# Kernel optimization log

Measured on AMD Instinct MI355X. Metric: run time of the kernel, lower is better.

The kernel has to match this reference:

```python
import jax, jax.numpy as jnp
import numpy as np

N_NODES = 50000
HIDDEN = 64
N_EDGES = 800000
HOPS = (1, 2, 3)


def setup_inputs() -> dict:
    key = jax.random.key(0)
    ks = jax.random.split(key, 16)
    d = HIDDEN
    inp = {
        "x": jax.random.normal(ks[0], (N_NODES, d), dtype=jnp.float32),
        "edge_index": jax.random.randint(ks[1], (2, N_EDGES), 0, N_NODES, dtype=jnp.int64),
    }
    s = 1.0 / np.sqrt(d)
    # per-hop GIN MLP params: Linear(d,d) -> ReLU -> Linear(d,d)
    for i in range(len(HOPS)):
        inp[f"W1_{i}"] = jax.random.uniform(ks[2 + 4 * i], (d, d), jnp.float32, -s, s)
        inp[f"b1_{i}"] = jax.random.uniform(ks[3 + 4 * i], (d,), jnp.float32, -s, s)
        inp[f"W2_{i}"] = jax.random.uniform(ks[4 + 4 * i], (d, d), jnp.float32, -s, s)
        inp[f"b2_{i}"] = jax.random.uniform(ks[5 + 4 * i], (d,), jnp.float32, -s, s)
    so = 1.0 / np.sqrt(d * len(HOPS))
    inp["Wo"] = jax.random.uniform(ks[14], (d * len(HOPS), d), jnp.float32, -so, so)
    inp["bo"] = jax.random.uniform(ks[15], (d,), jnp.float32, -so, so)
    return inp


def _gin_conv(h, src, dst, W1, b1, W2, b2):
    # GINConv with eps=0: MLP(x + sum_{j in N(i)} x_j)
    agg = jax.ops.segment_sum(h[src], dst, num_segments=N_NODES)  # [N, d]
    z = h + agg
    z = jax.nn.relu(z @ W1 + b1) @ W2 + b2
    return z


def reference(x, edge_index,
              W1_0, b1_0, W2_0, b2_0,
              W1_1, b1_1, W2_1, b2_1,
              W1_2, b1_2, W2_2, b2_2,
              Wo, bo):
    src, dst = edge_index[0], edge_index[1]
    params = [(W1_0, b1_0, W2_0, b2_0),
              (W1_1, b1_1, W2_1, b2_1),
              (W1_2, b1_2, W2_2, b2_2)]
    outs = []
    for hop, (W1, b1, W2, b2) in zip(HOPS, params):
        h = x
        for _ in range(hop):
            h = _gin_conv(h, src, dst, W1, b1, W2, b2)
        outs.append(h)
    return jnp.concatenate(outs, axis=-1) @ Wo + bo
```

## Files before the change

kernel.cpp:

```cpp
#include <hip/hip_runtime.h>

#define NN 50000
#define NE 800000
#define D  64
#define TILE 64
#define TPB 512
#define NBLK 196


__global__ __launch_bounds__(256) void k_count(const int* __restrict__ ei, int* __restrict__ deg) {
    int e = blockIdx.x * 256 + threadIdx.x;
    if (e < NE) atomicAdd(&deg[ei[NE + e]], 1);
}

__global__ __launch_bounds__(256) void k_scan2(const int* __restrict__ deg,
                                               int* __restrict__ row_ptr,
                                               int* __restrict__ cursor) {
    __shared__ int s[256];
    __shared__ int sboff;
    int t = threadIdx.x;
    int b = blockIdx.x;

    int lim = b * 256;
    int pacc = 0;
    for (int i = t; i < lim; i += 256) pacc += deg[i];
    s[t] = pacc;
    __syncthreads();
    for (int off = 128; off > 0; off >>= 1) {
        if (t < off) s[t] += s[t + off];
        __syncthreads();
    }
    if (t == 0) sboff = s[0];
    __syncthreads();
    int boffv = sboff;
    __syncthreads();

    int i = lim + t;
    int v = (i < NN) ? deg[i] : 0;
    s[t] = v;
    __syncthreads();
    for (int off = 1; off < 256; off <<= 1) {
        int u = (t >= off) ? s[t - off] : 0;
        __syncthreads();
        s[t] += u;
        __syncthreads();
    }
    int excl = s[t] - v + boffv;
    if (i < NN) { row_ptr[i] = excl; cursor[i] = excl; }
    if (b == 0 && t == 0) row_ptr[NN] = NE;
}

__global__ __launch_bounds__(256) void k_fill(const int* __restrict__ ei,
                                              int* __restrict__ cursor,
                                              int* __restrict__ colv) {
    int e = blockIdx.x * 256 + threadIdx.x;
    if (e < NE) {
        int d = ei[NE + e];
        int p = atomicAdd(&cursor[d], 1);
        colv[p] = ei[e];
    }
}


__device__ __forceinline__ float4 gather_row(const float4* __restrict__ h4,
                                             const int* __restrict__ row_ptr,
                                             const int* __restrict__ colv,
                                             int n, int g, int q) {
    float4 a0 = make_float4(0.f, 0.f, 0.f, 0.f);
    float4 a1 = make_float4(0.f, 0.f, 0.f, 0.f);
    float4 a2 = make_float4(0.f, 0.f, 0.f, 0.f);
    float4 a3 = make_float4(0.f, 0.f, 0.f, 0.f);
    if (n >= 0) {
        if (g == 0) a0 = h4[n * 16 + q];
        int e1 = row_ptr[n + 1];
        int e  = row_ptr[n] + g;
        for (; e + 12 < e1; e += 16) {
            int s0 = colv[e], s1 = colv[e + 4], s2 = colv[e + 8], s3 = colv[e + 12];
            float4 v0 = h4[s0 * 16 + q];
            float4 v1 = h4[s1 * 16 + q];
            float4 v2 = h4[s2 * 16 + q];
            float4 v3 = h4[s3 * 16 + q];
            a0.x += v0.x; a0.y += v0.y; a0.z += v0.z; a0.w += v0.w;
            a1.x += v1.x; a1.y += v1.y; a1.z += v1.z; a1.w += v1.w;
            a2.x += v2.x; a2.y += v2.y; a2.z += v2.z; a2.w += v2.w;
            a3.x += v3.x; a3.y += v3.y; a3.z += v3.z; a3.w += v3.w;
        }
        for (; e < e1; e += 4) {
            float4 v = h4[colv[e] * 16 + q];
            a1.x += v.x; a1.y += v.y; a1.z += v.z; a1.w += v.w;
        }
        a0.x += a1.x + a2.x + a3.x;
        a0.y += a1.y + a2.y + a3.y;
        a0.z += a1.z + a2.z + a3.z;
        a0.w += a1.w + a2.w + a3.w;
    }
    a0.x += __shfl_xor(a0.x, 16); a0.y += __shfl_xor(a0.y, 16);
    a0.z += __shfl_xor(a0.z, 16); a0.w += __shfl_xor(a0.w, 16);
    a0.x += __shfl_xor(a0.x, 32); a0.y += __shfl_xor(a0.y, 32);
    a0.z += __shfl_xor(a0.z, 32); a0.w += __shfl_xor(a0.w, 32);
    return a0;
}


__device__ __forceinline__ void conv_body(
    const float4* __restrict__ h4,
    const int* __restrict__ row_ptr,
    const int* __restrict__ colv,
    const float* __restrict__ W1, const float* __restrict__ b1,
    const float* __restrict__ W2, const float* __restrict__ b2,
    float4* __restrict__ out4,
    float (&sW)[D][D], float4 (&sZ4)[TILE][17], float* sB1, float* sB2,
    int node0)
{
    int tid = threadIdx.x;

    {
        const float4* w14 = (const float4*)W1;
        float4* s14 = (float4*)sW;
        for (int i = tid; i < D * D / 4; i += TPB) s14[i] = w14[i];
        if (tid < D) { sB1[tid] = b1[tid]; sB2[tid] = b2[tid]; }
    }

    int wave = tid >> 6, lane = tid & 63;
    int g = lane >> 4, q = lane & 15;

    for (int r = wave; r < TILE; r += (TPB / 64)) {
        int n = node0 + r;
        float4 a = gather_row(h4, row_ptr, colv, (n < NN) ? n : -1, g, q);
        if (g == 0) sZ4[r][q] = a;
    }
    __syncthreads();

    int tr = tid >> 4, tc = tid & 15;
    float* zr0 = (float*)&sZ4[tr * 2 + 0][0];
    float* zr1 = (float*)&sZ4[tr * 2 + 1][0];

    float acc[2][4];
    #pragma unroll
    for (int c = 0; c < 4; ++c) { acc[0][c] = sB1[tc * 4 + c]; acc[1][c] = sB1[tc * 4 + c]; }
    #pragma unroll 16
    for (int k = 0; k < D; ++k) {
        float z0 = zr0[k], z1 = zr1[k];
        #pragma unroll
        for (int c = 0; c < 4; ++c) {
            float w = sW[k][tc * 4 + c];
            acc[0][c] += z0 * w;
            acc[1][c] += z1 * w;
        }
    }
    {
        float4 h0, h1;
        h0.x = fmaxf(acc[0][0], 0.f); h0.y = fmaxf(acc[0][1], 0.f);
        h0.z = fmaxf(acc[0][2], 0.f); h0.w = fmaxf(acc[0][3], 0.f);
        h1.x = fmaxf(acc[1][0], 0.f); h1.y = fmaxf(acc[1][1], 0.f);
        h1.z = fmaxf(acc[1][2], 0.f); h1.w = fmaxf(acc[1][3], 0.f);
        *(float4*)&zr0[tc * 4] = h0;
        *(float4*)&zr1[tc * 4] = h1;
    }
    __syncthreads();

    {
        const float4* w24 = (const float4*)W2;
        float4* s24 = (float4*)sW;
        for (int i = tid; i < D * D / 4; i += TPB) s24[i] = w24[i];
    }
    __syncthreads();

    #pragma unroll
    for (int c = 0; c < 4; ++c) { acc[0][c] = sB2[tc * 4 + c]; acc[1][c] = sB2[tc * 4 + c]; }
    #pragma unroll 16
    for (int k = 0; k < D; ++k) {
        float z0 = zr0[k], z1 = zr1[k];
        #pragma unroll
        for (int c = 0; c < 4; ++c) {
            float w = sW[k][tc * 4 + c];
            acc[0][c] += z0 * w;
            acc[1][c] += z1 * w;
        }
    }
    #pragma unroll
    for (int i = 0; i < 2; ++i) {
        int n = node0 + tr * 2 + i;
        if (n < NN) {
            float4 o;
            o.x = acc[i][0]; o.y = acc[i][1]; o.z = acc[i][2]; o.w = acc[i][3];
            out4[n * 16 + tc] = o;
        }
    }
}

__global__ __launch_bounds__(TPB, 8) void k_conv_dual(
    const float4* __restrict__ hA4, const float4* __restrict__ hB4,
    const int* __restrict__ row_ptr,
    const int* __restrict__ colv,
    const float* __restrict__ W1a, const float* __restrict__ b1a,
    const float* __restrict__ W2a, const float* __restrict__ b2a,
    const float* __restrict__ W1b, const float* __restrict__ b1b,
    const float* __restrict__ W2b, const float* __restrict__ b2b,
    float4* __restrict__ outA4, float4* __restrict__ outB4, int nb)
{
    __shared__ float sW[D][D];
    __shared__ float4 sZ4[TILE][17];
    __shared__ float sB1[D], sB2[D];
    int b = blockIdx.x;
    if (b < nb) {
        conv_body(hA4, row_ptr, colv, W1a, b1a, W2a, b2a, outA4,
                  sW, sZ4, sB1, sB2, b * TILE);
    } else {
        conv_body(hB4, row_ptr, colv, W1b, b1b, W2b, b2b, outB4,
                  sW, sZ4, sB1, sB2, (b - nb) * TILE);
    }
}


__global__ __launch_bounds__(TPB, 8) void k_conv_last(
    const float4* __restrict__ h4,
    const float4* __restrict__ H0, const float4* __restrict__ H1,
    const int* __restrict__ row_ptr, const int* __restrict__ colv,
    const float* __restrict__ W1, const float* __restrict__ b1,
    const float* __restrict__ W2, const float* __restrict__ b2,
    const float* __restrict__ Wo, const float* __restrict__ bo,
    float4* __restrict__ out4)
{
    __shared__ float sW[D][D];
    __shared__ float4 sZ4[TILE][17];
    __shared__ float sB1[D], sB2[D];

    int tid = threadIdx.x;
    int node0 = blockIdx.x * TILE;

    {
        const float4* w14 = (const float4*)W1;
        float4* s14 = (float4*)sW;
        for (int i = tid; i < D * D / 4; i += TPB) s14[i] = w14[i];
        if (tid < D) { sB1[tid] = b1[tid]; sB2[tid] = b2[tid]; }
    }

    int wave = tid >> 6, lane = tid & 63;
    int g = lane >> 4, q = lane & 15;

    for (int r = wave; r < TILE; r += (TPB / 64)) {
        int n = node0 + r;
        float4 a = gather_row(h4, row_ptr, colv, (n < NN) ? n : -1, g, q);
        if (g == 0) sZ4[r][q] = a;
    }
    __syncthreads();

    int tr = tid >> 4, tc = tid & 15;
    float* zr0 = (float*)&sZ4[tr * 2 + 0][0];
    float* zr1 = (float*)&sZ4[tr * 2 + 1][0];

    float acc[2][4];
    #pragma unroll
    for (int c = 0; c < 4; ++c) { acc[0][c] = sB1[tc * 4 + c]; acc[1][c] = sB1[tc * 4 + c]; }
    #pragma unroll 16
    for (int k = 0; k < D; ++k) {
        float z0 = zr0[k], z1 = zr1[k];
        #pragma unroll
        for (int c = 0; c < 4; ++c) {
            float w = sW[k][tc * 4 + c];
            acc[0][c] += z0 * w;
            acc[1][c] += z1 * w;
        }
    }
    {
        float4 h0, h1;
        h0.x = fmaxf(acc[0][0], 0.f); h0.y = fmaxf(acc[0][1], 0.f);
        h0.z = fmaxf(acc[0][2], 0.f); h0.w = fmaxf(acc[0][3], 0.f);
        h1.x = fmaxf(acc[1][0], 0.f); h1.y = fmaxf(acc[1][1], 0.f);
        h1.z = fmaxf(acc[1][2], 0.f); h1.w = fmaxf(acc[1][3], 0.f);
        *(float4*)&zr0[tc * 4] = h0;
        *(float4*)&zr1[tc * 4] = h1;
    }
    __syncthreads();

    {
        const float4* w24 = (const float4*)W2;
        float4* s24 = (float4*)sW;
        for (int i = tid; i < D * D / 4; i += TPB) s24[i] = w24[i];
    }
    __syncthreads();

    #pragma unroll
    for (int c = 0; c < 4; ++c) { acc[0][c] = sB2[tc * 4 + c]; acc[1][c] = sB2[tc * 4 + c]; }
    #pragma unroll 16
    for (int k = 0; k < D; ++k) {
        float z0 = zr0[k], z1 = zr1[k];
        #pragma unroll
        for (int c = 0; c < 4; ++c) {
            float w = sW[k][tc * 4 + c];
            acc[0][c] += z0 * w;
            acc[1][c] += z1 * w;
        }
    }
    {
        float4 h0, h1;
        h0.x = acc[0][0]; h0.y = acc[0][1]; h0.z = acc[0][2]; h0.w = acc[0][3];
        h1.x = acc[1][0]; h1.y = acc[1][1]; h1.z = acc[1][2]; h1.w = acc[1][3];
        *(float4*)&zr0[tc * 4] = h0;
        *(float4*)&zr1[tc * 4] = h1;
    }
    __syncthreads();

    float accO[2][4];
    int n0 = node0 + tr * 2 + 0;
    int n1 = node0 + tr * 2 + 1;

    #pragma unroll 1
    for (int m = 0; m < 3; ++m) {
        {
            const float4* w4 = (const float4*)(Wo + m * 64 * D);
            float4* s4 = (float4*)sW;
            for (int i = tid; i < D * D / 4; i += TPB) s4[i] = w4[i];
        }
        __syncthreads();

        if (m == 0) {
            #pragma unroll
            for (int c = 0; c < 4; ++c) { accO[0][c] = sB1[0] * 0.f; }
            #pragma unroll
            for (int c = 0; c < 4; ++c) { accO[0][c] = bo[tc * 4 + c]; accO[1][c] = accO[0][c]; }
        }

        if (m < 2) {
            const float4* Hc = (m == 0) ? H0 : H1;
            #pragma unroll 4
            for (int k4 = 0; k4 < 16; ++k4) {
                float4 z0v = Hc[n0 * 16 + k4];
                float4 z1v = Hc[n1 * 16 + k4];
                #pragma unroll
                for (int j = 0; j < 4; ++j) {
                    int k = k4 * 4 + j;
                    float z0 = (j == 0) ? z0v.x : (j == 1) ? z0v.y : (j == 2) ? z0v.z : z0v.w;
                    float z1 = (j == 0) ? z1v.x : (j == 1) ? z1v.y : (j == 2) ? z1v.z : z1v.w;
                    #pragma unroll
                    for (int c = 0; c < 4; ++c) {
                        float w = sW[k][tc * 4 + c];
                        accO[0][c] += z0 * w;
                        accO[1][c] += z1 * w;
                    }
                }
            }
        } else {
            #pragma unroll 16
            for (int k = 0; k < D; ++k) {
                float z0 = zr0[k], z1 = zr1[k];
                #pragma unroll
                for (int c = 0; c < 4; ++c) {
                    float w = sW[k][tc * 4 + c];
                    accO[0][c] += z0 * w;
                    accO[1][c] += z1 * w;
                }
            }
        }
        if (m < 2) __syncthreads();
    }

    #pragma unroll
    for (int i = 0; i < 2; ++i) {
        int n = node0 + tr * 2 + i;
        if (n < NN) {
            float4 o;
            o.x = accO[i][0]; o.y = accO[i][1]; o.z = accO[i][2]; o.w = accO[i][3];
            out4[n * 16 + tc] = o;
        }
    }
}


__global__ __launch_bounds__(TPB) void k_aggmlp3(
    const float4* __restrict__ h4,
    const int* __restrict__ row_ptr,
    const int* __restrict__ colv,
    const float* __restrict__ W1a, const float* __restrict__ b1a,
    const float* __restrict__ W2a, const float* __restrict__ b2a,
    const float* __restrict__ W1b, const float* __restrict__ b1b,
    const float* __restrict__ W2b, const float* __restrict__ b2b,
    const float* __restrict__ W1c, const float* __restrict__ b1c,
    const float* __restrict__ W2c, const float* __restrict__ b2c,
    float4* __restrict__ outA, float4* __restrict__ outB, float4* __restrict__ outC)
{
    __shared__ float sW[D][D];
    __shared__ float4 sZ4[TILE][17];
    __shared__ float4 sH4[TILE][17];
    __shared__ float sB[D];

    int tid = threadIdx.x;
    int node0 = blockIdx.x * TILE;

    int wave = tid >> 6, lane = tid & 63;
    int g = lane >> 4, q = lane & 15;

    for (int r = wave; r < TILE; r += (TPB / 64)) {
        int n = node0 + r;
        float4 a = gather_row(h4, row_ptr, colv, (n < NN) ? n : -1, g, q);
        if (g == 0) sZ4[r][q] = a;
    }

    int tr = tid >> 4, tc = tid & 15;
    float* zr0 = (float*)&sZ4[tr * 2 + 0][0];
    float* zr1 = (float*)&sZ4[tr * 2 + 1][0];
    float* hr0 = (float*)&sH4[tr * 2 + 0][0];
    float* hr1 = (float*)&sH4[tr * 2 + 1][0];

    #pragma unroll 1
    for (int m = 0; m < 3; ++m) {
        const float* W1 = (m == 0) ? W1a : (m == 1) ? W1b : W1c;
        const float* B1 = (m == 0) ? b1a : (m == 1) ? b1b : b1c;
        const float* W2 = (m == 0) ? W2a : (m == 1) ? W2b : W2c;
        const float* B2 = (m == 0) ? b2a : (m == 1) ? b2b : b2c;
        float4* out4 = (m == 0) ? outA : (m == 1) ? outB : outC;

        {
            const float4* w4 = (const float4*)W1;
            float4* s4 = (float4*)sW;
            for (int i = tid; i < D * D / 4; i += TPB) s4[i] = w4[i];
            if (tid < D) sB[tid] = B1[tid];
        }
        __syncthreads();

        float acc[2][4];
        #pragma unroll
        for (int c = 0; c < 4; ++c) { acc[0][c] = sB[tc * 4 + c]; acc[1][c] = sB[tc * 4 + c]; }
        #pragma unroll 16
        for (int k = 0; k < D; ++k) {
            float z0 = zr0[k], z1 = zr1[k];
            #pragma unroll
            for (int c = 0; c < 4; ++c) {
                float w = sW[k][tc * 4 + c];
                acc[0][c] += z0 * w;
                acc[1][c] += z1 * w;
            }
        }
        {
            float4 h0, h1;
            h0.x = fmaxf(acc[0][0], 0.f); h0.y = fmaxf(acc[0][1], 0.f);
            h0.z = fmaxf(acc[0][2], 0.f); h0.w = fmaxf(acc[0][3], 0.f);
            h1.x = fmaxf(acc[1][0], 0.f); h1.y = fmaxf(acc[1][1], 0.f);
            h1.z = fmaxf(acc[1][2], 0.f); h1.w = fmaxf(acc[1][3], 0.f);
            *(float4*)&hr0[tc * 4] = h0;
            *(float4*)&hr1[tc * 4] = h1;
        }
        __syncthreads();

        {
            const float4* w4 = (const float4*)W2;
            float4* s4 = (float4*)sW;
            for (int i = tid; i < D * D / 4; i += TPB) s4[i] = w4[i];
            if (tid < D) sB[tid] = B2[tid];
        }
        __syncthreads();

        #pragma unroll
        for (int c = 0; c < 4; ++c) { acc[0][c] = sB[tc * 4 + c]; acc[1][c] = sB[tc * 4 + c]; }
        #pragma unroll 16
        for (int k = 0; k < D; ++k) {
            float h0 = hr0[k], h1 = hr1[k];
            #pragma unroll
            for (int c = 0; c < 4; ++c) {
                float w = sW[k][tc * 4 + c];
                acc[0][c] += h0 * w;
                acc[1][c] += h1 * w;
            }
        }
        #pragma unroll
        for (int i = 0; i < 2; ++i) {
            int n = node0 + tr * 2 + i;
            if (n < NN) {
                float4 o;
                o.x = acc[i][0]; o.y = acc[i][1]; o.z = acc[i][2]; o.w = acc[i][3];
                out4[n * 16 + tc] = o;
            }
        }
        __syncthreads();
    }
}


extern "C" void kernel_launch(void* const* d_in, const int* in_sizes, int n_in,
                              void* d_out, int out_size, void* d_ws, size_t ws_size,
                              hipStream_t stream) {
    const float* x    = (const float*)d_in[0];
    const int*   ei   = (const int*)d_in[1];
    const float* W1_0 = (const float*)d_in[2];
    const float* b1_0 = (const float*)d_in[3];
    const float* W2_0 = (const float*)d_in[4];
    const float* b2_0 = (const float*)d_in[5];
    const float* W1_1 = (const float*)d_in[6];
    const float* b1_1 = (const float*)d_in[7];
    const float* W2_1 = (const float*)d_in[8];
    const float* b2_1 = (const float*)d_in[9];
    const float* W1_2 = (const float*)d_in[10];
    const float* b1_2 = (const float*)d_in[11];
    const float* W2_2 = (const float*)d_in[12];
    const float* b2_2 = (const float*)d_in[13];
    const float* Wo   = (const float*)d_in[14];
    const float* bo   = (const float*)d_in[15];
    float4* out = (float4*)d_out;

    char* ws = (char*)d_ws;
    int* deg     = (int*)(ws + 0);
    int* cursor  = (int*)(ws + 200704);
    int* row_ptr = (int*)(ws + 401408);
    int* colv    = (int*)(ws + 602112);
    float* fbase = (float*)(ws + 3804160);
    float4* H0  = (float4*)(fbase);
    float4* H1  = (float4*)(fbase + 3200000);
    float4* tB  = (float4*)(fbase + 6400000);
    float4* tC2 = (float4*)(fbase + 9600000);
    const float4* x4 = (const float4*)x;

    hipMemsetAsync(deg, 0, NN * sizeof(int), stream);
    k_count<<<(NE + 255) / 256, 256, 0, stream>>>(ei, deg);
    k_scan2<<<NBLK, 256, 0, stream>>>(deg, row_ptr, cursor);
    k_fill <<<(NE + 255) / 256, 256, 0, stream>>>(ei, cursor, colv);

    int nb = (NN + TILE - 1) / TILE;

    k_aggmlp3<<<nb, TPB, 0, stream>>>(x4, row_ptr, colv,
                                      W1_0, b1_0, W2_0, b2_0,
                                      W1_1, b1_1, W2_1, b2_1,
                                      W1_2, b1_2, W2_2, b2_2,
                                      H0, tB, out);

    k_conv_dual<<<2 * nb, TPB, 0, stream>>>(
        (const float4*)tB, (const float4*)out, row_ptr, colv,
        W1_1, b1_1, W2_1, b2_1,
        W1_2, b1_2, W2_2, b2_2,
        H1, tC2, nb);

    k_conv_last<<<nb, TPB, 0, stream>>>((const float4*)tC2,
                                        (const float4*)H0, (const float4*)H1,
                                        row_ptr, colv,
                                        W1_2, b1_2, W2_2, b2_2,
                                        Wo, bo, out);
}
```

Measured before the change: 371.4 us.

## Fuse whole MixHop pipeline into one cooperative persistent kernel with grid syncs

Replaces the multi-kernel sequence (degree count, scan, fill, aggregation+MLP, dual conv, last conv) with a single cooperative launch of 782 blocks that separates the phases with grid.sync(). This removes per-kernel launch gaps and lets the CSR build and the three hops run inside one resident grid. It keeps a fallback to separate kernels, which now split the last conv and the output projection into k_conv and k_final. It depends on all 782 blocks of 512 threads fitting co-resident; if they do not, the cooperative launch fails and the fallback runs. The fused path also adds full-grid barriers, extra round trips of the aggregated features through global memory, and a first-hop MLP whose three weight sets run serially per block.

New measurement: 1.007 ms. 171% more time.

```diff
diff --git a/kernel.cpp b/kernel.cpp
--- a/kernel.cpp
+++ b/kernel.cpp
@@ -1,65 +1,16 @@
 #include <hip/hip_runtime.h>
+#include <hip/hip_cooperative_groups.h>
+
+namespace cg = cooperative_groups;
 
 #define NN 50000
 #define NE 800000
 #define D  64
 #define TILE 64
 #define TPB 512
+#define NBG 782
+#define NSB 98
 #define NBLK 196
-
-
-__global__ __launch_bounds__(256) void k_count(const int* __restrict__ ei, int* __restrict__ deg) {
-    int e = blockIdx.x * 256 + threadIdx.x;
-    if (e < NE) atomicAdd(&deg[ei[NE + e]], 1);
-}
-
-__global__ __launch_bounds__(256) void k_scan2(const int* __restrict__ deg,
-                                               int* __restrict__ row_ptr,
-                                               int* __restrict__ cursor) {
-    __shared__ int s[256];
-    __shared__ int sboff;
-    int t = threadIdx.x;
-    int b = blockIdx.x;
-
-    int lim = b * 256;
-    int pacc = 0;
-    for (int i = t; i < lim; i += 256) pacc += deg[i];
-    s[t] = pacc;
-    __syncthreads();
-    for (int off = 128; off > 0; off >>= 1) {
-        if (t < off) s[t] += s[t + off];
-        __syncthreads();
-    }
-    if (t == 0) sboff = s[0];
-    __syncthreads();
-    int boffv = sboff;
-    __syncthreads();
-
-    int i = lim + t;
-    int v = (i < NN) ? deg[i] : 0;
-    s[t] = v;
-    __syncthreads();
-    for (int off = 1; off < 256; off <<= 1) {
-        int u = (t >= off) ? s[t - off] : 0;
-        __syncthreads();
-        s[t] += u;
-        __syncthreads();
-    }
-    int excl = s[t] - v + boffv;
-    if (i < NN) { row_ptr[i] = excl; cursor[i] = excl; }
-    if (b == 0 && t == 0) row_ptr[NN] = NE;
-}
-
-__global__ __launch_bounds__(256) void k_fill(const int* __restrict__ ei,
-                                              int* __restrict__ cursor,
-                                              int* __restrict__ colv) {
-    int e = blockIdx.x * 256 + threadIdx.x;
-    if (e < NE) {
-        int d = ei[NE + e];
-        int p = atomicAdd(&cursor[d], 1);
-        colv[p] = ei[e];
-    }
-}
 
 
 __device__ __forceinline__ float4 gather_row(const float4* __restrict__ h4,
@@ -187,6 +138,301 @@
             out4[n * 16 + tc] = o;
         }
     }
+    __syncthreads();
+}
+
+
+__global__ __launch_bounds__(TPB, 8) void k_mixhop(
+    const float4* __restrict__ x4, const int* __restrict__ ei,
+    const float* __restrict__ W1_0, const float* __restrict__ b1_0,
+    const float* __restrict__ W2_0, const float* __restrict__ b2_0,
+    const float* __restrict__ W1_1, const float* __restrict__ b1_1,
+    const float* __restrict__ W2_1, const float* __restrict__ b2_1,
+    const float* __restrict__ W1_2, const float* __restrict__ b1_2,
+    const float* __restrict__ W2_2, const float* __restrict__ b2_2,
+    const float* __restrict__ Wo, const float* __restrict__ bo,
+    float4* __restrict__ out,
+    int* __restrict__ deg, int* __restrict__ cursor,
+    int* __restrict__ row_ptr, int* __restrict__ colv,
+    float4* __restrict__ H0, float4* __restrict__ H1,
+    float4* __restrict__ tB, float4* __restrict__ tC2)
+{
+    cg::grid_group grid = cg::this_grid();
+
+    __shared__ float sW[D][D];
+    __shared__ float4 sZ4[TILE][17];
+    __shared__ float sB1[D], sB2[D];
+
+    int tid = threadIdx.x;
+    int b = blockIdx.x;
+    int gsize = NBG * TPB;
+    int gtid = b * TPB + tid;
+    int node0 = b * TILE;
+
+    for (int i = gtid; i < NN; i += gsize) deg[i] = 0;
+    if (gtid == 0) row_ptr[NN] = NE;
+    grid.sync();
+
+    for (int e = gtid; e < NE; e += gsize) atomicAdd(&deg[ei[NE + e]], 1);
+    grid.sync();
+
+    if (b < NSB) {
+        int* s = (int*)sW;
+        int lim = b * TPB;
+        int pacc = 0;
+        for (int i = tid; i < lim; i += TPB) pacc += deg[i];
+        s[tid] = pacc;
+        __syncthreads();
+        for (int off = 256; off > 0; off >>= 1) {
+            if (tid < off) s[tid] += s[tid + off];
+            __syncthreads();
+        }
+        if (tid == 0) s[TPB] = s[0];
+        __syncthreads();
+        int boffv = s[TPB];
+        __syncthreads();
+
+        int i = lim + tid;
+        int v = (i < NN) ? deg[i] : 0;
+        s[tid] = v;
+        __syncthreads();
+        for (int off = 1; off < TPB; off <<= 1) {
+            int u = (tid >= off) ? s[tid - off] : 0;
+            __syncthreads();
+            s[tid] += u;
+            __syncthreads();
+        }
+        int excl = s[tid] - v + boffv;
+        if (i < NN) { row_ptr[i] = excl; cursor[i] = excl; }
+    }
+    grid.sync();
+
+    for (int e = gtid; e < NE; e += gsize) {
+        int dd = ei[NE + e];
+        int p = atomicAdd(&cursor[dd], 1);
+        colv[p] = ei[e];
+    }
+    grid.sync();
+
+    {
+        int wave = tid >> 6, lane = tid & 63;
+        int g = lane >> 4, q = lane & 15;
+        for (int r = wave; r < TILE; r += (TPB / 64)) {
+            int n = node0 + r;
+            float4 a = gather_row(x4, row_ptr, colv, (n < NN) ? n : -1, g, q);
+            if (g == 0 && n < NN) tC2[n * 16 + q] = a;
+        }
+    }
+    grid.sync();
+
+    {
+        int tr = tid >> 4, tc = tid & 15;
+        float* zr0 = (float*)&sZ4[tr * 2 + 0][0];
+        float* zr1 = (float*)&sZ4[tr * 2 + 1][0];
+
+        #pragma unroll 1
+        for (int m = 0; m < 3; ++m) {
+            const float* W1 = (m == 0) ? W1_0 : (m == 1) ? W1_1 : W1_2;
+            const float* B1 = (m == 0) ? b1_0 : (m == 1) ? b1_1 : b1_2;
+            const float* W2 = (m == 0) ? W2_0 : (m == 1) ? W2_1 : W2_2;
+            const float* B2 = (m == 0) ? b2_0 : (m == 1) ? b2_1 : b2_2;
+            float4* o4      = (m == 0) ? H0   : (m == 1) ? tB   : out;
+
+            {
+                const float4* w4 = (const float4*)W1;
+                float4* s4 = (float4*)sW;
+                for (int i = tid; i < D * D / 4; i += TPB) s4[i] = w4[i];
+                if (tid < D) { sB1[tid] = B1[tid]; sB2[tid] = B2[tid]; }
+            }
+            for (int i = tid; i < TILE * 16; i += TPB) {
+                int r = i >> 4, qq = i & 15;
+                int n = node0 + r;
+                sZ4[r][qq] = (n < NN) ? tC2[n * 16 + qq] : make_float4(0.f, 0.f, 0.f, 0.f);
+            }
+            __syncthreads();
+
+            float acc[2][4];
+            #pragma unroll
+            for (int c = 0; c < 4; ++c) { acc[0][c] = sB1[tc * 4 + c]; acc[1][c] = sB1[tc * 4 + c]; }
+            #pragma unroll 16
+            for (int k = 0; k < D; ++k) {
+                float z0 = zr0[k], z1 = zr1[k];
+                #pragma unroll
+                for (int c = 0; c < 4; ++c) {
+                    float w = sW[k][tc * 4 + c];
+                    acc[0][c] += z0 * w;
+                    acc[1][c] += z1 * w;
+                }
+            }
+            {
+                float4 h0, h1;
+                h0.x = fmaxf(acc[0][0], 0.f); h0.y = fmaxf(acc[0][1], 0.f);
+                h0.z = fmaxf(acc[0][2], 0.f); h0.w = fmaxf(acc[0][3], 0.f);
+                h1.x = fmaxf(acc[1][0], 0.f); h1.y = fmaxf(acc[1][1], 0.f);
+                h1.z = fmaxf(acc[1][2], 0.f); h1.w = fmaxf(acc[1][3], 0.f);
+                *(float4*)&zr0[tc * 4] = h0;
+                *(float4*)&zr1[tc * 4] = h1;
+            }
+            __syncthreads();
+
+            {
+                const float4* w4 = (const float4*)W2;
+                float4* s4 = (float4*)sW;
+                for (int i = tid; i < D * D / 4; i += TPB) s4[i] = w4[i];
+            }
+            __syncthreads();
+
+            #pragma unroll
+            for (int c = 0; c < 4; ++c) { acc[0][c] = sB2[tc * 4 + c]; acc[1][c] = sB2[tc * 4 + c]; }
+            #pragma unroll 16
+            for (int k = 0; k < D; ++k) {
+                float z0 = zr0[k], z1 = zr1[k];
+                #pragma unroll
+                for (int c = 0; c < 4; ++c) {
+                    float w = sW[k][tc * 4 + c];
+                    acc[0][c] += z0 * w;
+                    acc[1][c] += z1 * w;
+                }
+            }
+            #pragma unroll
+            for (int i = 0; i < 2; ++i) {
+                int n = node0 + tr * 2 + i;
+                if (n < NN) {
+                    float4 o;
+                    o.x = acc[i][0]; o.y = acc[i][1]; o.z = acc[i][2]; o.w = acc[i][3];
+                    o4[n * 16 + tc] = o;
+                }
+            }
+            __syncthreads();
+        }
+    }
+    grid.sync();
+
+    conv_body(tB,  row_ptr, colv, W1_1, b1_1, W2_1, b2_1, H1,  sW, sZ4, sB1, sB2, node0);
+    conv_body(out, row_ptr, colv, W1_2, b1_2, W2_2, b2_2, tC2, sW, sZ4, sB1, sB2, node0);
+    grid.sync();
+
+    conv_body(tC2, row_ptr, colv, W1_2, b1_2, W2_2, b2_2, tB, sW, sZ4, sB1, sB2, node0);
+    grid.sync();
+
+    {
+        int tr = tid >> 4, tc = tid & 15;
+        const float* yr0 = (const float*)&sZ4[tr * 2 + 0][0];
+        const float* yr1 = (const float*)&sZ4[tr * 2 + 1][0];
+        float accO[2][4];
+
+        #pragma unroll 1
+        for (int m = 0; m < 3; ++m) {
+            const float4* Hc = (m == 0) ? H0 : (m == 1) ? H1 : tB;
+            {
+                const float4* w4 = (const float4*)(Wo + m * 64 * D);
+                float4* s4 = (float4*)sW;
+                for (int i = tid; i < D * D / 4; i += TPB) s4[i] = w4[i];
+                if (m == 0 && tid < D) sB1[tid] = bo[tid];
+            }
+            for (int i = tid; i < TILE * 16; i += TPB) {
+                int r = i >> 4, qq = i & 15;
+                int n = node0 + r;
+                sZ4[r][qq] = (n < NN) ? Hc[n * 16 + qq] : make_float4(0.f, 0.f, 0.f, 0.f);
+            }
+            __syncthreads();
+
+            if (m == 0) {
+                #pragma unroll
+                for (int c = 0; c < 4; ++c) { accO[0][c] = sB1[tc * 4 + c]; accO[1][c] = sB1[tc * 4 + c]; }
+            }
+            #pragma unroll 16
+            for (int k = 0; k < D; ++k) {
+                float z0 = yr0[k], z1 = yr1[k];
+                #pragma unroll
+                for (int c = 0; c < 4; ++c) {
+                    float w = sW[k][tc * 4 + c];
+                    accO[0][c] += z0 * w;
+                    accO[1][c] += z1 * w;
+                }
+            }
+            __syncthreads();
+        }
+
+        #pragma unroll
+        for (int i = 0; i < 2; ++i) {
+            int n = node0 + tr * 2 + i;
+            if (n < NN) {
+                float4 o;
+                o.x = accO[i][0]; o.y = accO[i][1]; o.z = accO[i][2]; o.w = accO[i][3];
+                out[n * 16 + tc] = o;
+            }
+        }
+    }
+}
+
+
+__global__ __launch_bounds__(256) void k_count(const int* __restrict__ ei, int* __restrict__ deg) {
+    int e = blockIdx.x * 256 + threadIdx.x;
+    if (e < NE) atomicAdd(&deg[ei[NE + e]], 1);
+}
+
+__global__ __launch_bounds__(256) void k_scan2(const int* __restrict__ deg,
+                                               int* __restrict__ row_ptr,
+                                               int* __restrict__ cursor) {
+    __shared__ int s[256];
+    __shared__ int sboff;
+    int t = threadIdx.x;
+    int b = blockIdx.x;
+
+    int lim = b * 256;
+    int pacc = 0;
+    for (int i = t; i < lim; i += 256) pacc += deg[i];
+    s[t] = pacc;
+    __syncthreads();
+    for (int off = 128; off > 0; off >>= 1) {
+        if (t < off) s[t] += s[t + off];
+        __syncthreads();
+    }
+    if (t == 0) sboff = s[0];
+    __syncthreads();
+    int boffv = sboff;
+    __syncthreads();
+
+    int i = lim + t;
+    int v = (i < NN) ? deg[i] : 0;
+    s[t] = v;
+    __syncthreads();
+    for (int off = 1; off < 256; off <<= 1) {
+        int u = (t >= off) ? s[t - off] : 0;
+        __syncthreads();
+        s[t] += u;
+        __syncthreads();
+    }
+    int excl = s[t] - v + boffv;
+    if (i < NN) { row_ptr[i] = excl; cursor[i] = excl; }
+    if (b == 0 && t == 0) row_ptr[NN] = NE;
+}
+
+__global__ __launch_bounds__(256) void k_fill(const int* __restrict__ ei,
+                                              int* __restrict__ cursor,
+                                              int* __restrict__ colv) {
+    int e = blockIdx.x * 256 + threadIdx.x;
+    if (e < NE) {
+        int d = ei[NE + e];
+        int p = atomicAdd(&cursor[d], 1);
+        colv[p] = ei[e];
+    }
+}
+
+__global__ __launch_bounds__(TPB, 8) void k_conv(
+    const float4* __restrict__ h4,
+    const int* __restrict__ row_ptr,
+    const int* __restrict__ colv,
+    const float* __restrict__ W1, const float* __restrict__ b1,
+    const float* __restrict__ W2, const float* __restrict__ b2,
+    float4* __restrict__ out4)
+{
+    __shared__ float sW[D][D];
+    __shared__ float4 sZ4[TILE][17];
+    __shared__ float sB1[D], sB2[D];
+    conv_body(h4, row_ptr, colv, W1, b1, W2, b2, out4,
+              sW, sZ4, sB1, sB2, blockIdx.x * TILE);
 }
 
 __global__ __launch_bounds__(TPB, 8) void k_conv_dual(
@@ -212,162 +458,6 @@
     }
 }
 
-
-__global__ __launch_bounds__(TPB, 8) void k_conv_last(
-    const float4* __restrict__ h4,
-    const float4* __restrict__ H0, const float4* __restrict__ H1,
-    const int* __restrict__ row_ptr, const int* __restrict__ colv,
-    const float* __restrict__ W1, const float* __restrict__ b1,
-    const float* __restrict__ W2, const float* __restrict__ b2,
-    const float* __restrict__ Wo, const float* __restrict__ bo,
-    float4* __restrict__ out4)
-{
-    __shared__ float sW[D][D];
-    __shared__ float4 sZ4[TILE][17];
-    __shared__ float sB1[D], sB2[D];
-
-    int tid = threadIdx.x;
-    int node0 = blockIdx.x * TILE;
-
-    {
-        const float4* w14 = (const float4*)W1;
-        float4* s14 = (float4*)sW;
-        for (int i = tid; i < D * D / 4; i += TPB) s14[i] = w14[i];
-        if (tid < D) { sB1[tid] = b1[tid]; sB2[tid] = b2[tid]; }
-    }
-
-    int wave = tid >> 6, lane = tid & 63;
-    int g = lane >> 4, q = lane & 15;
-
-    for (int r = wave; r < TILE; r += (TPB / 64)) {
-        int n = node0 + r;
-        float4 a = gather_row(h4, row_ptr, colv, (n < NN) ? n : -1, g, q);
-        if (g == 0) sZ4[r][q] = a;
-    }
-    __syncthreads();
-
-    int tr = tid >> 4, tc = tid & 15;
-    float* zr0 = (float*)&sZ4[tr * 2 + 0][0];
-    float* zr1 = (float*)&sZ4[tr * 2 + 1][0];
-
-    float acc[2][4];
-    #pragma unroll
-    for (int c = 0; c < 4; ++c) { acc[0][c] = sB1[tc * 4 + c]; acc[1][c] = sB1[tc * 4 + c]; }
-    #pragma unroll 16
-    for (int k = 0; k < D; ++k) {
-        float z0 = zr0[k], z1 = zr1[k];
-        #pragma unroll
-        for (int c = 0; c < 4; ++c) {
-            float w = sW[k][tc * 4 + c];
-            acc[0][c] += z0 * w;
-            acc[1][c] += z1 * w;
-        }
-    }
-    {
-        float4 h0, h1;
-        h0.x = fmaxf(acc[0][0], 0.f); h0.y = fmaxf(acc[0][1], 0.f);
-        h0.z = fmaxf(acc[0][2], 0.f); h0.w = fmaxf(acc[0][3], 0.f);
-        h1.x = fmaxf(acc[1][0], 0.f); h1.y = fmaxf(acc[1][1], 0.f);
-        h1.z = fmaxf(acc[1][2], 0.f); h1.w = fmaxf(acc[1][3], 0.f);
-        *(float4*)&zr0[tc * 4] = h0;
-        *(float4*)&zr1[tc * 4] = h1;
-    }
-    __syncthreads();
-
-    {
-        const float4* w24 = (const float4*)W2;
-        float4* s24 = (float4*)sW;
-        for (int i = tid; i < D * D / 4; i += TPB) s24[i] = w24[i];
-    }
-    __syncthreads();
-
-    #pragma unroll
-    for (int c = 0; c < 4; ++c) { acc[0][c] = sB2[tc * 4 + c]; acc[1][c] = sB2[tc * 4 + c]; }
-    #pragma unroll 16
-    for (int k = 0; k < D; ++k) {
-        float z0 = zr0[k], z1 = zr1[k];
-        #pragma unroll
-        for (int c = 0; c < 4; ++c) {
-            float w = sW[k][tc * 4 + c];
-            acc[0][c] += z0 * w;
-            acc[1][c] += z1 * w;
-        }
-    }
-    {
-        float4 h0, h1;
-        h0.x = acc[0][0]; h0.y = acc[0][1]; h0.z = acc[0][2]; h0.w = acc[0][3];
-        h1.x = acc[1][0]; h1.y = acc[1][1]; h1.z = acc[1][2]; h1.w = acc[1][3];
-        *(float4*)&zr0[tc * 4] = h0;
-        *(float4*)&zr1[tc * 4] = h1;
-    }
-    __syncthreads();
-
-    float accO[2][4];
-    int n0 = node0 + tr * 2 + 0;
-    int n1 = node0 + tr * 2 + 1;
-
-    #pragma unroll 1
-    for (int m = 0; m < 3; ++m) {
-        {
-            const float4* w4 = (const float4*)(Wo + m * 64 * D);
-            float4* s4 = (float4*)sW;
-            for (int i = tid; i < D * D / 4; i += TPB) s4[i] = w4[i];
-        }
-        __syncthreads();
-
-        if (m == 0) {
-            #pragma unroll
-            for (int c = 0; c < 4; ++c) { accO[0][c] = sB1[0] * 0.f; }
-            #pragma unroll
-            for (int c = 0; c < 4; ++c) { accO[0][c] = bo[tc * 4 + c]; accO[1][c] = accO[0][c]; }
-        }
-
-        if (m < 2) {
-            const float4* Hc = (m == 0) ? H0 : H1;
-            #pragma unroll 4
-            for (int k4 = 0; k4 < 16; ++k4) {
-                float4 z0v = Hc[n0 * 16 + k4];
-                float4 z1v = Hc[n1 * 16 + k4];
-                #pragma unroll
-                for (int j = 0; j < 4; ++j) {
-                    int k = k4 * 4 + j;
-                    float z0 = (j == 0) ? z0v.x : (j == 1) ? z0v.y : (j == 2) ? z0v.z : z0v.w;
-                    float z1 = (j == 0) ? z1v.x : (j == 1) ? z1v.y : (j == 2) ? z1v.z : z1v.w;
-                    #pragma unroll
-                    for (int c = 0; c < 4; ++c) {
-                        float w = sW[k][tc * 4 + c];
-                        accO[0][c] += z0 * w;
-                        accO[1][c] += z1 * w;
-                    }
-                }
-            }
-        } else {
-            #pragma unroll 16
-            for (int k = 0; k < D; ++k) {
-                float z0 = zr0[k], z1 = zr1[k];
-                #pragma unroll
-                for (int c = 0; c < 4; ++c) {
-                    float w = sW[k][tc * 4 + c];
-                    accO[0][c] += z0 * w;
-                    accO[1][c] += z1 * w;
-                }
-            }
-        }
-        if (m < 2) __syncthreads();
-    }
-
-    #pragma unroll
-    for (int i = 0; i < 2; ++i) {
-        int n = node0 + tr * 2 + i;
-        if (n < NN) {
-            float4 o;
-            o.x = accO[i][0]; o.y = accO[i][1]; o.z = accO[i][2]; o.w = accO[i][3];
-            out4[n * 16 + tc] = o;
-        }
-    }
-}
-
-
 __global__ __launch_bounds__(TPB) void k_aggmlp3(
     const float4* __restrict__ h4,
     const int* __restrict__ row_ptr,
@@ -476,12 +566,74 @@
     }
 }
 
+__global__ __launch_bounds__(TPB, 8) void k_final(
+    const float4* __restrict__ H0, const float4* __restrict__ H1,
+    const float4* __restrict__ H2,
+    const float* __restrict__ Wo, const float* __restrict__ bo,
+    float4* __restrict__ out4)
+{
+    __shared__ float sW[D][D];
+    __shared__ float4 sY4[TILE][17];
+    __shared__ float sB[D];
+
+    int tid = threadIdx.x;
+    int node0 = blockIdx.x * TILE;
+    int tr = tid >> 4, tc = tid & 15;
+    const float* yr0 = (const float*)&sY4[tr * 2 + 0][0];
+    const float* yr1 = (const float*)&sY4[tr * 2 + 1][0];
+
+    float accO[2][4];
+
+    #pragma unroll 1
+    for (int m = 0; m < 3; ++m) {
+        const float4* Hc = (m == 0) ? H0 : (m == 1) ? H1 : H2;
+        {
+            const float4* w4 = (const float4*)(Wo + m * 64 * D);
+            float4* s4 = (float4*)sW;
+            for (int i = tid; i < D * D / 4; i += TPB) s4[i] = w4[i];
+            if (m == 0 && tid < D) sB[tid] = bo[tid];
+        }
+        for (int i = tid; i < TILE * 16; i += TPB) {
+            int r = i >> 4, qq = i & 15;
+            int n = node0 + r;
+            sY4[r][qq] = (n < NN) ? Hc[n * 16 + qq] : make_float4(0.f, 0.f, 0.f, 0.f);
+        }
+        __syncthreads();
+
+        if (m == 0) {
+            #pragma unroll
+            for (int c = 0; c < 4; ++c) { accO[0][c] = sB[tc * 4 + c]; accO[1][c] = sB[tc * 4 + c]; }
+        }
+        #pragma unroll 16
+        for (int k = 0; k < D; ++k) {
+            float z0 = yr0[k], z1 = yr1[k];
+            #pragma unroll
+            for (int c = 0; c < 4; ++c) {
+                float w = sW[k][tc * 4 + c];
+                accO[0][c] += z0 * w;
+                accO[1][c] += z1 * w;
+            }
+        }
+        __syncthreads();
+    }
+
+    #pragma unroll
+    for (int i = 0; i < 2; ++i) {
+        int n = node0 + tr * 2 + i;
+        if (n < NN) {
+            float4 o;
+            o.x = accO[i][0]; o.y = accO[i][1]; o.z = accO[i][2]; o.w = accO[i][3];
+            out4[n * 16 + tc] = o;
+        }
+    }
+}
+
 
 extern "C" void kernel_launch(void* const* d_in, const int* in_sizes, int n_in,
                               void* d_out, int out_size, void* d_ws, size_t ws_size,
                               hipStream_t stream) {
-    const float* x    = (const float*)d_in[0];
-    const int*   ei   = (const int*)d_in[1];
+    const float4* x4  = (const float4*)d_in[0];
+    const int*    ei  = (const int*)d_in[1];
     const float* W1_0 = (const float*)d_in[2];
     const float* b1_0 = (const float*)d_in[3];
     const float* W2_0 = (const float*)d_in[4];
@@ -508,7 +660,21 @@
     float4* H1  = (float4*)(fbase + 3200000);
     float4* tB  = (float4*)(fbase + 6400000);
     float4* tC2 = (float4*)(fbase + 9600000);
-    const float4* x4 = (const float4*)x;
+
+    void* args[] = {
+        (void*)&x4, (void*)&ei,
+        (void*)&W1_0, (void*)&b1_0, (void*)&W2_0, (void*)&b2_0,
+        (void*)&W1_1, (void*)&b1_1, (void*)&W2_1, (void*)&b2_1,
+        (void*)&W1_2, (void*)&b1_2, (void*)&W2_2, (void*)&b2_2,
+        (void*)&Wo, (void*)&bo,
+        (void*)&out,
+        (void*)&deg, (void*)&cursor, (void*)&row_ptr, (void*)&colv,
+        (void*)&H0, (void*)&H1, (void*)&tB, (void*)&tC2
+    };
+    hipError_t rc = hipLaunchCooperativeKernel((const void*)k_mixhop, dim3(NBG), dim3(TPB),
+                                               args, 0, stream);
+    if (rc == hipSuccess) return;
+    (void)hipGetLastError();
 
     hipMemsetAsync(deg, 0, NN * sizeof(int), stream);
     k_count<<<(NE + 255) / 256, 256, 0, stream>>>(ei, deg);
@@ -524,14 +690,14 @@
                                       H0, tB, out);
 
     k_conv_dual<<<2 * nb, TPB, 0, stream>>>(
-        (const float4*)tB, (const float4*)out, row_ptr, colv,
+        tB, (const float4*)out, row_ptr, colv,
         W1_1, b1_1, W2_1, b2_1,
         W1_2, b1_2, W2_2, b2_2,
         H1, tC2, nb);
 
-    k_conv_last<<<nb, TPB, 0, stream>>>((const float4*)tC2,
-                                        (const float4*)H0, (const float4*)H1,
-                                        row_ptr, colv,
-                                        W1_2, b1_2, W2_2, b2_2,
-                                        Wo, bo, out);
-}
+    k_conv<<<nb, TPB, 0, stream>>>((const float4*)tC2, row_ptr, colv,
+                                   W1_2, b1_2, W2_2, b2_2, tB);
+
+    k_final<<<nb, TPB, 0, stream>>>((const float4*)H0, (const float4*)H1, (const float4*)tB,
+                                    Wo, bo, out);
+}
```
